# Performance work log

Hardware: AMD Instinct MI355X
Metric: run time of the kernel (lower is better)

The kernel has to match this reference:

```python
import jax, jax.numpy as jnp
import numpy as np

B, T, S, R, L = 16, 32, 512, 8, 256
H, E, V, NL = 512, 512, 50000, 3
OOV = 50


def setup_inputs() -> dict:
    key = jax.random.key(0)
    ks = jax.random.split(key, 40)
    p = lambda i, shape: jax.random.normal(ks[i], shape, dtype=jnp.float32) * 0.02
    d = {
        'tokens': jax.random.randint(ks[0], (B, T), 0, V),
        'src_oov': jax.random.randint(ks[1], (B, S), 0, V),
        'ref_oovs': jax.random.randint(ks[2], (B, R, L), 0, V),
        'src_mask': jnp.ones((B, S), bool),
        'ref_word_mask': jnp.ones((B, R, L), bool),
        'ref_doc_mask': jnp.ones((B, R), bool),
        'max_num_oov': OOV,
        'cur_word_rep': jax.random.normal(ks[3], (B, S, H), dtype=jnp.float32),
        'ref_word_reps': jax.random.normal(ks[4], (B, R, L, H), dtype=jnp.float32),
        'ref_doc_reps': jax.random.normal(ks[5], (B, R, H), dtype=jnp.float32),
        'hidden0': jax.random.normal(ks[6], (NL, B, H), dtype=jnp.float32),
        'embed_w': p(7, (V, E)),
        'gru_wih': p(8, (NL, 3 * H, H)),  # layer0 input dim E == H
        'gru_whh': p(9, (NL, 3 * H, H)),
        'gru_bih': p(10, (NL, 3 * H)),
        'gru_bhh': p(11, (NL, 3 * H)),
        'attn_Wd': p(12, (H, H)), 'attn_We': p(13, (H, H)), 'attn_v': p(14, (H,)),
        'hd_Wd': p(15, (H, H)), 'hd_We': p(16, (H, H)), 'hd_v': p(17, (H,)),
        'hw_Wd': p(18, (H, H)), 'hw_We': p(19, (H, H)), 'hw_v': p(20, (H,)),
        'gate_w': p(21, (2 * H, 1)), 'gate_b': p(22, (1,)),
        'fc_w': p(23, (2 * H, H)), 'fc_b': p(24, (H,)),
        'out_w': p(25, (H, V)), 'out_b': p(26, (V,)),
        'pgen_w': p(27, (E + 2 * H, 3)), 'pgen_b': p(28, (3,)),
    }
    return d


def _forward(embed_w, gru_wih, gru_whh, gru_bih, gru_bhh,
             attn_Wd, attn_We, attn_v, hd_Wd, hd_We, hd_v, hw_Wd, hw_We, hw_v,
             gate_w, gate_b, fc_w, fc_b, out_w, out_b, pgen_w, pgen_b,
             cur_word_rep, ref_word_reps, ref_doc_reps, hidden0,
             tokens, src_oov, ref_oovs, src_mask, ref_word_mask, ref_doc_mask,
             max_num_oov):
    b, t = tokens.shape
    x = embed_w[tokens]                               # [B,T,E]
    enc_proj = cur_word_rep @ attn_We                 # [B,S,H]
    doc_proj = ref_doc_reps @ hd_We                   # [B,R,H]
    word_proj = ref_word_reps @ hw_We                 # [B,R,L,H]
    NEG = jnp.float32(-1e9)

    def step(hidden, x_t):
        inp = x_t
        hs = []
        for l in range(hidden.shape[0]):
            gx = inp @ gru_wih[l].T + gru_bih[l]
            gh = hidden[l] @ gru_whh[l].T + gru_bhh[l]
            xr, xz, xn = jnp.split(gx, 3, -1)
            hr, hz, hn = jnp.split(gh, 3, -1)
            r = jax.nn.sigmoid(xr + hr)
            z = jax.nn.sigmoid(xz + hz)
            n = jnp.tanh(xn + r * hn)
            h = (1.0 - z) * n + z * hidden[l]
            hs.append(h)
            inp = h
        new_hidden = jnp.stack(hs)
        h_top = hs[-1]                                # [B,H]
        # additive attention over source words
        sc = jnp.tanh(enc_proj + (h_top @ attn_Wd)[:, None, :]) @ attn_v  # [B,S]
        aw = jax.nn.softmax(jnp.where(src_mask, sc, NEG), -1)
        ctx = jnp.einsum('bs,bsh->bh', aw, cur_word_rep)
        # hierarchical attention: doc level then word level
        scd = jnp.tanh(doc_proj + (h_top @ hd_Wd)[:, None, :]) @ hd_v     # [B,R]
        ad = jax.nn.softmax(jnp.where(ref_doc_mask, scd, NEG), -1)
        scw = jnp.tanh(word_proj + (h_top @ hw_Wd)[:, None, None, :]) @ hw_v  # [B,R,L]
        aww = jax.nn.softmax(jnp.where(ref_word_mask, scw, NEG), -1)
        ra = ad[:, :, None] * aww                     # [B,R,L]
        rctx = jnp.einsum('brl,brlh->bh', ra, ref_word_reps)
        # fusion gate
        g = jax.nn.sigmoid(jnp.concatenate([ctx, rctx], -1) @ gate_w + gate_b)  # [B,1]
        context = g * ctx + (1.0 - g) * rctx
        return new_hidden, (context, h_top, aw, ra)

    _, (contexts, hiddens, attn_dists, ref_attn_dists) = jax.lax.scan(
        step, hidden0, jnp.swapaxes(x, 0, 1))
    contexts = jnp.swapaxes(contexts, 0, 1)           # [B,T,H]
    hiddens = jnp.swapaxes(hiddens, 0, 1)             # [B,T,H]
    attn_dists = jnp.swapaxes(attn_dists, 0, 1)       # [B,T,S]
    ref_attn_dists = jnp.swapaxes(ref_attn_dists, 0, 1)  # [B,T,R,L]

    ch = jnp.concatenate([contexts, hiddens], -1)
    vocab_dist = jax.nn.softmax((ch @ fc_w + fc_b) @ out_w + out_b, -1)  # [B,T,V]
    pg = jax.nn.softmax(jnp.concatenate([contexts, hiddens, x], -1) @ pgen_w + pgen_b, -1)  # [B,T,3]
    vocab_dist_ = pg[..., 0:1] * vocab_dist
    attn_ = pg[..., 1:2] * attn_dists
    final = jnp.concatenate(
        [vocab_dist_, jnp.zeros((b, t, max_num_oov), vocab_dist_.dtype)], -1)
    bi = jnp.arange(b)[:, None, None]
    ti = jnp.arange(t)[None, :, None]
    idx = jnp.broadcast_to(src_oov[:, None, :], (b, t, src_oov.shape[-1]))
    final = final.at[bi, ti, idx].add(attn_)
    # multi-doc copy
    r, l = ref_oovs.shape[1], ref_oovs.shape[2]
    ref_attn_ = pg[..., 2][:, :, None, None] * ref_attn_dists
    ridx = jnp.broadcast_to(ref_oovs.reshape(b, 1, r * l), (b, t, r * l))
    final = final.at[bi, ti, ridx].add(ref_attn_.reshape(b, t, r * l))
    return final, attn_dists


def reference(tokens, src_oov, ref_oovs, src_mask, ref_word_mask, ref_doc_mask,
              max_num_oov, cur_word_rep, ref_word_reps, ref_doc_reps, hidden0,
              embed_w, gru_wih, gru_whh, gru_bih, gru_bhh,
              attn_Wd, attn_We, attn_v, hd_Wd, hd_We, hd_v, hw_Wd, hw_We, hw_v,
              gate_w, gate_b, fc_w, fc_b, out_w, out_b, pgen_w, pgen_b):
    return _forward(embed_w, gru_wih, gru_whh, gru_bih, gru_bhh,
                    attn_Wd, attn_We, attn_v, hd_Wd, hd_We, hd_v,
                    hw_Wd, hw_We, hw_v, gate_w, gate_b, fc_w, fc_b,
                    out_w, out_b, pgen_w, pgen_b,
                    cur_word_rep, ref_word_reps, ref_doc_reps, hidden0,
                    tokens, src_oov, ref_oovs, src_mask, ref_word_mask,
                    ref_doc_mask, max_num_oov)
```

## Files before the change

kernel.cpp:

```cpp
#include <hip/hip_runtime.h>
#include <hip/hip_bf16.h>


#define B_   16
#define T_   32
#define S_   512
#define R_   8
#define L_   256
#define RL_  2048
#define H_   512
#define V_   50000
#define NL_  3
#define OOV_ 50
#define M_   512
#define FINW 50050
#define S2C  2.8853900817779268f
#define GRUB 128
#define NCONV 128
#define HP16 520

typedef __attribute__((ext_vector_type(8))) short    short8;
typedef __attribute__((ext_vector_type(4))) float    f32x4;
typedef __attribute__((ext_vector_type(2))) _Float16 h2;
typedef __attribute__((ext_vector_type(8))) _Float16 h8;
// ... 32 lines not shown
__device__ __forceinline__ float dot8h(h8 w, h8 x, float acc){
#if __has_builtin(__builtin_amdgcn_fdot2)
  acc = __builtin_amdgcn_fdot2((h2){w[0], w[1]}, (h2){x[0], x[1]}, acc, false);
  acc = __builtin_amdgcn_fdot2((h2){w[2], w[3]}, (h2){x[2], x[3]}, acc, false);
  acc = __builtin_amdgcn_fdot2((h2){w[4], w[5]}, (h2){x[4], x[5]}, acc, false);
  acc = __builtin_amdgcn_fdot2((h2){w[6], w[7]}, (h2){x[6], x[7]}, acc, false);
#else
  #pragma unroll
  for (int q = 0; q < 8; q++) acc += (float)w[q] * (float)x[q];
#endif
  return acc;
}
__device__ __forceinline__ u64 allc(const u64* p){
  return __hip_atomic_load(p, __ATOMIC_RELAXED, __HIP_MEMORY_SCOPE_AGENT);
}
__device__ __forceinline__ float allcf(const float* p){
  u32 v = __hip_atomic_load((const u32*)p, __ATOMIC_RELAXED, __HIP_MEMORY_SCOPE_AGENT);
  union { u32 i; float f; } c; c.i = v; return c.f;
}


__global__ __launch_bounds__(256) void k_embed(const int* __restrict__ tokens,
                                               const float* __restrict__ embed_w,
                                               u16* __restrict__ x_bf){
  int rid = blockIdx.x;
  long tok = (long)tokens[rid];
  const float* src = embed_w + tok * H_;
  u16* dst = x_bf + (long)rid * H_;
  for (int e = threadIdx.x; e < H_; e += 256) dst[e] = f2bf(src[e]);
}

struct CJ { const float* s; u16* d; long n; int f16; };

__global__ __launch_bounds__(256) void k_conv6(CJ j0, CJ j1, CJ j2, CJ j3, CJ j4, CJ j5){
  int y = blockIdx.y;
  CJ j = (y == 0) ? j0 : (y == 1) ? j1 : (y == 2) ? j2 : (y == 3) ? j3 : (y == 4) ? j4 : j5;
  long n4 = j.n >> 2;
  long i = (long)blockIdx.x * 256 + threadIdx.x;
  long stride = (long)gridDim.x * 256;
  if (j.f16){
    for (; i < n4; i += stride){
      f32x4 v = *(const f32x4*)(j.s + 4 * i);
      u64 p = (u64)f2h(v[0]) | ((u64)f2h(v[1]) << 16)
            | ((u64)f2h(v[2]) << 32) | ((u64)f2h(v[3]) << 48);
      *(u64*)(j.d + 4 * i) = p;
    }
  } else {
    for (; i < n4; i += stride){
      f32x4 v = *(const f32x4*)(j.s + 4 * i);
      u64 p = (u64)f2bf(v[0]) | ((u64)f2bf(v[1]) << 16)
            | ((u64)f2bf(v[2]) << 32) | ((u64)f2bf(v[3]) << 48);
      *(u64*)(j.d + 4 * i) = p;
    }
  }
}

__global__ __launch_bounds__(256) void k_convT(const float* __restrict__ src, int Rr, int Cc,
                                               u16* __restrict__ dst){
  __shared__ float tile[32][33];
  int c0 = blockIdx.x * 32, r0 = blockIdx.y * 32;
  int tx = threadIdx.x & 31, ty = threadIdx.x >> 5;
  for (int i = ty; i < 32; i += 8){
    int r = r0 + i, c = c0 + tx;
    tile[i][tx] = (r < Rr && c < Cc) ? src[(long)r * Cc + c] : 0.f;
  }
  __syncthreads();
  for (int i = ty; i < 32; i += 8){
    int c = c0 + i, r = r0 + tx;
    if (c < Cc && r < Rr) dst[(long)c * Rr + r] = f2bf(tile[tx][i]);
  }
}

__global__ __launch_bounds__(256) void k_convT6(const float* s0, const float* s1,
    const float* s2, const float* s3, const float* s4, const float* s5,
    u16* __restrict__ dstb){
  int z = blockIdx.z;
  const float* src = (z == 0) ? s0 : (z == 1) ? s1 : (z == 2) ? s2
                   : (z == 3) ? s3 : (z == 4) ? s4 : s5;
  u16* dst = dstb + (long)z * H_ * H_;
  __shared__ float tile[32][33];
  int c0 = blockIdx.x * 32, r0 = blockIdx.y * 32;
  int tx = threadIdx.x & 31, ty = threadIdx.x >> 5;
  for (int i = ty; i < 32; i += 8)
    tile[i][tx] = src[(long)(r0 + i) * H_ + c0 + tx];
  __syncthreads();
  for (int i = ty; i < 32; i += 8)
// ... 149 lines not shown
  float mp = -1e30f;
  #pragma unroll 8
  for (int k = 0; k < 64; k += 2){
    float x0 = cbuf[rl][cbase + k], x1 = cbuf[rl][cbase + k + 1];
    float2 xy; xy.x = x0; xy.y = x1;
    *(float2*)(fin + gbase + k) = xy;
    if (cg + k < N)     mp = fmaxf(mp, x0);
    if (cg + k + 1 < N) mp = fmaxf(mp, x1);
  }
  float sp = 0.f;
  #pragma unroll 8
  for (int k = 0; k < 64; k++){
    if (cg + k < N) sp += __expf(cbuf[rl][cbase + k] - mp);
  }
  smx[rl][ch] = mp; ssx[rl][ch] = sp;
  __syncthreads();
  if (tid < 128){
    float ma = smx[tid][0], mb2 = smx[tid][1];
    float M = fmaxf(ma, mb2);
    float S = ssx[tid][0] * __expf(ma - M) + ssx[tid][1] * __expf(mb2 - M);
    long row = mb + tid;
    pm[row * 392 + blockIdx.y] = M;
    ps[row * 392 + blockIdx.y] = S;
  }
}


__global__ __launch_bounds__(512) void k_gru_mega(
    const float* __restrict__ gx0, const u16* __restrict__ wih_h,
    const u16* __restrict__ whh_h, const float* __restrict__ bih,
    const float* __restrict__ bhh, const float* __restrict__ hidden0,
    float* __restrict__ h_all, u16* __restrict__ ch_bf, unsigned int* cnt,
    const float* __restrict__ out_w, u16* __restrict__ outwT,
    const u16* __restrict__ cwr_bf, const u16* __restrict__ rwr_bf,
    const u16* __restrict__ rdr_bf, const u16* __restrict__ WT,
    u16* __restrict__ enc_bf, u16* __restrict__ wp_bf,
    float* __restrict__ doc_proj, int do_shadow){
  __shared__ u16 pH0[16][HP16], pH1[16][HP16], pX1[16][HP16], pH2[16][HP16], pX2[16][HP16];
  __shared__ float red0[8][3][4][16];
  __shared__ float red1[8][6][4][16];
  __shared__ float red2[8][6][4][16];
  __shared__ float tconv[2][32][33];
  int bid = blockIdx.x;
  int tid = threadIdx.x;

  if (bid >= GRUB){
    if (!do_shadow) return;
    int wid = bid - GRUB;
    int half = tid >> 8, t256 = tid & 255;
    int worker = wid * 2 + half;
    for (int tile = worker; tile < 1284; tile += 256){
      if (tile < 256)
        dev_gemm_tile(cwr_bf, H_, WT, H_, (const float*)0, (void*)enc_bf, H_,
                      H_, H_, 1, S2C, tile >> 2, tile & 3, t256);
      else if (tile < 1280){
        int t = tile - 256;
        dev_gemm_tile(rwr_bf, H_, WT + 2 * H_ * H_, H_, (const float*)0, (void*)wp_bf, H_,
                      H_, H_, 1, S2C, t >> 2, t & 3, t256);
      } else
        dev_gemm_tile(rdr_bf, H_, WT + H_ * H_, H_, (const float*)0, (void*)doc_proj, H_,
                      H_, H_, 0, S2C, 0, tile - 1280, t256);
    }
    __syncthreads();
    int sub = half, tx = t256 & 31, ty = t256 >> 5;
    const int NT = 1563 * 16;
    for (int base = wid * 2; base < NT; base += NCONV * 2){
      int tile = base + sub;
      bool act = tile < NT;
      int cx = act ? (tile % 1563) : 0;
      int ry = act ? (tile / 1563) : 0;
      int c0 = cx * 32, r0 = ry * 32;
      if (act){
        for (int i = ty; i < 32; i += 8){
          int c = c0 + tx;
          tconv[sub][i][tx] = (c < V_) ? out_w[(long)(r0 + i) * V_ + c] : 0.f;
        }
      }
      __syncthreads();
      if (act){
        for (int i = ty; i < 32; i += 8){
          int c = c0 + i;
          if (c < V_) outwT[(long)c * H_ + r0 + tx] = f2bf(tconv[sub][tx][i]);
        }
      }
      __syncthreads();
    }
    return;
  }

  int bx = bid;
  int b = tid & 15, jj = (tid >> 4) & 3, ks = tid >> 6;
  int j = bx * 4 + jj;
  int kbase = ks * 64;
  int srow = tid >> 5, sl32 = tid & 31;

  for (int s = 0; s < T_ + NL_ - 1; s++){
    int t0 = s, t1 = s - 1, t2v = s - 2;
    bool a0 = (t0 < T_);
    bool a1 = (t1 >= 0 && t1 < T_);
    bool a2 = (t2v >= 0 && t2v < T_);
    float hpj_r = 0.f, gx_r0 = 0.f, gx_r1 = 0.f, gx_r2 = 0.f;
    if (tid < 192){
      int lz = tid >> 6, b2 = tid & 15, jj2 = (tid >> 4) & 3;
      int j2 = bx * 4 + jj2;
      int tt = s - lz;
      if (tt >= 0 && tt < T_){
        hpj_r = (tt == 0) ? hidden0[(lz * B_ + b2) * H_ + j2]
                          : allcf(h_all + (long)((lz * T_ + tt - 1) * B_ + b2) * H_ + j2);
        if (lz == 0){
          const float* g = gx0 + (long)(b2 * T_ + tt) * 1536 + j2;
          gx_r0 = g[0]; gx_r1 = g[512]; gx_r2 = g[1024];
        }
      }
    }
    {
      u64 v;
      #define STAGE(PAN, ROWPTR, ATOMIC)                                         \
        {                                                                        \
          const u64* p = (const u64*)(ROWPTR);                                   \
          _Pragma("unroll")                                                      \
          for (int q = 0; q < 8; q++){                                           \
            v = (ATOMIC) ? allc(p + sl32 + 32 * q) : p[sl32 + 32 * q];           \
            union { u64 w; float f[2]; } uu; uu.w = v;                           \
            union { _Float16 h[2]; u32 u; } pk;                                  \
            pk.h[0] = (_Float16)uu.f[0]; pk.h[1] = (_Float16)uu.f[1];            \
            *(u32*)&PAN[srow][2 * (sl32 + 32 * q)] = pk.u;                       \
          }                                                                      \
        }
      if (a0){
        if (t0 == 0) STAGE(pH0, hidden0 + (long)(0 * B_ + srow) * H_, false)
        else         STAGE(pH0, h_all + (long)((0 * T_ + t0 - 1) * B_ + srow) * H_, true)
      }
      if (a1){
        if (t1 == 0) STAGE(pH1, hidden0 + (long)(1 * B_ + srow) * H_, false)
        else         STAGE(pH1, h_all + (long)((1 * T_ + t1 - 1) * B_ + srow) * H_, true)
        STAGE(pX1, h_all + (long)((0 * T_ + t1) * B_ + srow) * H_, true)
      }
      if (a2){
        if (t2v == 0) STAGE(pH2, hidden0 + (long)(2 * B_ + srow) * H_, false)
        else          STAGE(pH2, h_all + (long)((2 * T_ + t2v - 1) * B_ + srow) * H_, true)
        STAGE(pX2, h_all + (long)((1 * T_ + t2v) * B_ + srow) * H_, true)
      }
      #undef STAGE
    }
    __syncthreads();

    if (a0){
      const u16* wl = whh_h;
      const h8* w0 = (const h8*)(wl + ((long)(0 * H_ + j)) * H_ + kbase);
      const h8* w1 = (const h8*)(wl + ((long)(1 * H_ + j)) * H_ + kbase);
      const h8* w2 = (const h8*)(wl + ((long)(2 * H_ + j)) * H_ + kbase);
      float s0 = 0.f, s1 = 0.f, s2 = 0.f;
      #pragma unroll 2
      for (int k8 = 0; k8 < 8; k8++){
        h8 hv = *(const h8*)&pH0[b][kbase + 8 * k8];
        s0 = dot8h(w0[k8], hv, s0);
        s1 = dot8h(w1[k8], hv, s1);
        s2 = dot8h(w2[k8], hv, s2);
      }
      red0[ks][0][jj][b] = s0; red0[ks][1][jj][b] = s1; red0[ks][2][jj][b] = s2;
    }
    if (a1){
      const u16* wl = whh_h + (long)1 * 1536 * H_;
      const u16* ul = wih_h + (long)1 * 1536 * H_;
      const h8* w0 = (const h8*)(wl + ((long)(0 * H_ + j)) * H_ + kbase);
      const h8* w1 = (const h8*)(wl + ((long)(1 * H_ + j)) * H_ + kbase);
      const h8* w2 = (const h8*)(wl + ((long)(2 * H_ + j)) * H_ + kbase);
      const h8* u0 = (const h8*)(ul + ((long)(0 * H_ + j)) * H_ + kbase);
      const h8* u1 = (const h8*)(ul + ((long)(1 * H_ + j)) * H_ + kbase);
      const h8* u2 = (const h8*)(ul + ((long)(2 * H_ + j)) * H_ + kbase);
      float s0 = 0.f, s1 = 0.f, s2 = 0.f, x0 = 0.f, x1 = 0.f, x2 = 0.f;
      #pragma unroll 2
      for (int k8 = 0; k8 < 8; k8++){
        h8 hv = *(const h8*)&pH1[b][kbase + 8 * k8];
        h8 xv = *(const h8*)&pX1[b][kbase + 8 * k8];
        s0 = dot8h(w0[k8], hv, s0);
        s1 = dot8h(w1[k8], hv, s1);
        s2 = dot8h(w2[k8], hv, s2);
        x0 = dot8h(u0[k8], xv, x0);
        x1 = dot8h(u1[k8], xv, x1);
        x2 = dot8h(u2[k8], xv, x2);
      }
      red1[ks][0][jj][b] = s0; red1[ks][1][jj][b] = s1; red1[ks][2][jj][b] = s2;
      red1[ks][3][jj][b] = x0; red1[ks][4][jj][b] = x1; red1[ks][5][jj][b] = x2;
    }
    if (a2){
      const u16* wl = whh_h + (long)2 * 1536 * H_;
      const u16* ul = wih_h + (long)2 * 1536 * H_;
      const h8* w0 = (const h8*)(wl + ((long)(0 * H_ + j)) * H_ + kbase);
      const h8* w1 = (const h8*)(wl + ((long)(1 * H_ + j)) * H_ + kbase);
      const h8* w2 = (const h8*)(wl + ((long)(2 * H_ + j)) * H_ + kbase);
      const h8* u0 = (const h8*)(ul + ((long)(0 * H_ + j)) * H_ + kbase);
      const h8* u1 = (const h8*)(ul + ((long)(1 * H_ + j)) * H_ + kbase);
      const h8* u2 = (const h8*)(ul + ((long)(2 * H_ + j)) * H_ + kbase);
      float s0 = 0.f, s1 = 0.f, s2 = 0.f, x0 = 0.f, x1 = 0.f, x2 = 0.f;
      #pragma unroll 2
      for (int k8 = 0; k8 < 8; k8++){
        h8 hv = *(const h8*)&pH2[b][kbase + 8 * k8];
        h8 xv = *(const h8*)&pX2[b][kbase + 8 * k8];
        s0 = dot8h(w0[k8], hv, s0);
        s1 = dot8h(w1[k8], hv, s1);
        s2 = dot8h(w2[k8], hv, s2);
        x0 = dot8h(u0[k8], xv, x0);
        x1 = dot8h(u1[k8], xv, x1);
        x2 = dot8h(u2[k8], xv, x2);
      }
      red2[ks][0][jj][b] = s0; red2[ks][1][jj][b] = s1; red2[ks][2][jj][b] = s2;
      red2[ks][3][jj][b] = x0; red2[ks][4][jj][b] = x1; red2[ks][5][jj][b] = x2;
    }
    __syncthreads();

    if (tid < 192){
      int lz = tid >> 6, b2 = tid & 15, jj2 = (tid >> 4) & 3;
      int j2 = bx * 4 + jj2;
      int tt = s - lz;
      if (tt >= 0 && tt < T_){
        float gh[3], gxv[3];
        #pragma unroll
        for (int g = 0; g < 3; g++){
          float a = 0.f, c = 0.f;
          if (lz == 0){
            #pragma unroll
            for (int q = 0; q < 8; q++) a += red0[q][g][jj2][b2];
          } else if (lz == 1){
            #pragma unroll
            for (int q = 0; q < 8; q++){ a += red1[q][g][jj2][b2]; c += red1[q][3 + g][jj2][b2]; }
          } else {
            #pragma unroll
            for (int q = 0; q < 8; q++){ a += red2[q][g][jj2][b2]; c += red2[q][3 + g][jj2][b2]; }
          }
          gh[g] = a + bhh[lz * 1536 + g * H_ + j2];
          if (lz == 0) gxv[g] = (g == 0) ? gx_r0 : (g == 1) ? gx_r1 : gx_r2;
// ... 126 lines not shown
    if (tid == 0){
      float m = -1e30f;
      for (int q = 0; q < 8; q++) m = fmaxf(m, red8[q][0]);
      float e[8], sum = 0.f;
      for (int q = 0; q < 8; q++){ e[q] = __expf(red8[q][0] - m); sum += e[q]; }
      float inv = 1.f / sum;
      for (int q = 0; q < 8; q++) ad[rid * R_ + q] = e[q] * inv;
    }
  }
}

__global__ __launch_bounds__(256) void k_aww_ra(float* __restrict__ raBuf,
                                                const float* __restrict__ ad){
  int rid = blockIdx.x, r = blockIdx.y, tid = threadIdx.x;
  float* row = raBuf + (long)rid * RL_ + r * L_;
  float x = row[tid];
  float m = x;
  for (int o = 32; o > 0; o >>= 1) m = fmaxf(m, __shfl_xor(m, o));
  __shared__ float red[4];
  if ((tid & 63) == 0) red[tid >> 6] = m;
  __syncthreads();
  m = fmaxf(fmaxf(red[0], red[1]), fmaxf(red[2], red[3]));
  float e = __expf(x - m);
  float s = e;
  for (int o = 32; o > 0; o >>= 1) s += __shfl_xor(s, o);
  __syncthreads();
  if ((tid & 63) == 0) red[tid >> 6] = s;
  __syncthreads();
  s = red[0] + red[1] + red[2] + red[3];
  row[tid] = (e / s) * ad[rid * R_ + r];
}


__global__ __launch_bounds__(256) void k_awgemm(const float* __restrict__ wts, int KS, int CH,
    const u16* __restrict__ Wbuf, float* __restrict__ pdst){
  int b = blockIdx.x, ht = blockIdx.y, kc = blockIdx.z;
  int tid = threadIdx.x;
  int hl = tid & 63, tq = tid >> 6;
  int h = ht * 256 + hl * 4;
  int base = kc * CH;
  float a[8][4];
  #pragma unroll
  for (int tt = 0; tt < 8; tt++)
    #pragma unroll
    for (int q = 0; q < 4; q++) a[tt][q] = 0.f;
  const float* wrow = wts + ((long)(b * T_) + tq * 8) * KS + base;
  for (int sl = 0; sl < CH; sl++){
    const u16* wp = Wbuf + ((long)b * KS + base + sl) * H_ + h;
    u32 p0 = *(const u32*)(wp);
    u32 p1 = *(const u32*)(wp + 2);
    float v0 = bf2f((u16)(p0 & 0xffff)), v1 = bf2f((u16)(p0 >> 16));
    float v2 = bf2f((u16)(p1 & 0xffff)), v3 = bf2f((u16)(p1 >> 16));
    #pragma unroll
    for (int tt = 0; tt < 8; tt++){
      float w = wrow[(long)tt * KS + sl];
      a[tt][0] += w * v0; a[tt][1] += w * v1;
      a[tt][2] += w * v2; a[tt][3] += w * v3;
    }
  }
  #pragma unroll
  for (int tt = 0; tt < 8; tt++){
    long o = (long)kc * (2 * M_ * H_) + ((long)(b * T_ + tq * 8 + tt)) * H_ + h;
    *(f32x4*)(pdst + o) = (f32x4){a[tt][0], a[tt][1], a[tt][2], a[tt][3]};
  }
}

__global__ __launch_bounds__(256) void k_red8(const float* __restrict__ pbuf,
                                              float* __restrict__ outp){
  long n = 2L * M_ * H_;
// ... 28 lines not shown
    contexts[(long)rid * H_ + h] = v;
    ch_bf[(long)rid * 1024 + h] = f2bf(v);
  }
  float p0 = 0.f, p1 = 0.f, p2 = 0.f;
  for (int k = tid; k < 1536; k += 256){
    float v;
    if (k < 512)       v = g * c[k] + (1.f - g) * rc[k];
    else if (k < 1024) v = h_all[((2 * T_ + t) * B_ + b) * H_ + (k - 512)];
    else               v = bf2f(x_bf[(long)rid * H_ + (k - 1024)]);
    p0 += v * pgen_w[k * 3 + 0];
    p1 += v * pgen_w[k * 3 + 1];
    p2 += v * pgen_w[k * 3 + 2];
  }
  for (int o = 32; o > 0; o >>= 1){
    p0 += __shfl_xor(p0, o); p1 += __shfl_xor(p1, o); p2 += __shfl_xor(p2, o);
  }
  __shared__ float r0[4], r1[4], r2[4];
  if ((tid & 63) == 0){ r0[tid >> 6] = p0; r1[tid >> 6] = p1; r2[tid >> 6] = p2; }
  __syncthreads();
  if (tid == 0){
    p0 = r0[0]+r0[1]+r0[2]+r0[3] + pgen_b[0];
    p1 = r1[0]+r1[1]+r1[2]+r1[3] + pgen_b[1];
    p2 = r2[0]+r2[1]+r2[2]+r2[3] + pgen_b[2];
    float m = fmaxf(p0, fmaxf(p1, p2));
    float e0 = __expf(p0 - m), e1 = __expf(p1 - m), e2 = __expf(p2 - m);
    float inv = 1.f / (e0 + e1 + e2);
    pg[rid * 3 + 0] = e0 * inv;
    pg[rid * 3 + 1] = e1 * inv;
    pg[rid * 3 + 2] = e2 * inv;
  }
}


__global__ __launch_bounds__(256) void k_vred391(const float* __restrict__ pm,
    const float* __restrict__ ps, float* __restrict__ vmax, float* __restrict__ vsum){
  int rid = blockIdx.x, tid = threadIdx.x;
  const float* mrow = pm + (long)rid * 392;
  const float* srow = ps + (long)rid * 392;
  float m = -1e30f, s = 0.f;
  for (int q = tid; q < 391; q += 256){
    float m2 = mrow[q], s2 = srow[q];
    float M = fmaxf(m, m2);
    s = s * __expf(m - M) + s2 * __expf(m2 - M);
    m = M;
  }
  for (int o = 32; o > 0; o >>= 1){
    float m2 = __shfl_xor(m, o), s2 = __shfl_xor(s, o);
    float M = fmaxf(m, m2);
    s = s * __expf(m - M) + s2 * __expf(m2 - M);
    m = M;
  }
  __shared__ float rm[4], rs[4];
  if ((tid & 63) == 0){ rm[tid >> 6] = m; rs[tid >> 6] = s; }
  __syncthreads();
  if (tid == 0){
    float Mx = rm[0], Sx = rs[0];
    for (int q = 1; q < 4; q++){
      float M2 = fmaxf(Mx, rm[q]);
      Sx = Sx * __expf(Mx - M2) + rs[q] * __expf(rm[q] - M2);
      Mx = M2;
    }
    vmax[rid] = Mx; vsum[rid] = Sx;
  }
}

__global__ __launch_bounds__(256) void k_final_vocab(float* __restrict__ fin,
    const float* __restrict__ vmax, const float* __restrict__ vsum,
    const float* __restrict__ pg){
  int rid = blockIdx.y;
  int v = (blockIdx.x * 256 + threadIdx.x) * 2;
  if (v >= FINW) return;
  long base = (long)rid * FINW;
  float scale = pg[rid * 3 + 0] / vsum[rid];
  float mx = vmax[rid];
  if (v + 1 < V_){
    float2* p = (float2*)(fin + base + v);
    float2 x = *p;
    x.x = __expf(x.x - mx) * scale;
    x.y = __expf(x.y - mx) * scale;
    *p = x;
  } else {
    for (int q = 0; q < 2 && v + q < FINW; q++){
      float x = fin[base + v + q];
      fin[base + v + q] = (v + q < V_) ? __expf(x - mx) * scale : 0.f;
    }
  }
}

__global__ __launch_bounds__(256) void k_scatter_src(float* __restrict__ fin,
    const float* __restrict__ aw, const float* __restrict__ pg,
    const int* __restrict__ src_oov){
  int rid = blockIdx.x, tid = threadIdx.x;
  int b = rid / T_;
  float p1 = pg[rid * 3 + 1];
  for (int s = tid; s < S_; s += 256){
    float val = p1 * aw[(long)rid * S_ + s];
    int idx = src_oov[b * S_ + s];
    atomicAdd(fin + (long)rid * FINW + idx, val);
  }
}

__global__ __launch_bounds__(256) void k_scatter_ref(float* __restrict__ fin,
    const float* __restrict__ raBuf, const float* __restrict__ pg,
    const int* __restrict__ ref_oovs){
  int rid = blockIdx.x, tid = threadIdx.x;
  int b = rid / T_;
  float p2 = pg[rid * 3 + 2];
  for (int i = tid; i < RL_; i += 256){
    float val = p2 * raBuf[(long)rid * RL_ + i];
    int idx = ref_oovs[b * RL_ + i];
    atomicAdd(fin + (long)rid * FINW + idx, val);
  }
}


extern "C" void kernel_launch(void* const* d_in, const int* in_sizes, int n_in,
                              void* d_out, int out_size, void* d_ws, size_t ws_size,
                              hipStream_t stream)
{
  (void)in_sizes; (void)n_in; (void)out_size;
  const int*   tokens   = (const int*)  d_in[0];
  const int*   src_oov  = (const int*)  d_in[1];
  const int*   ref_oovs = (const int*)  d_in[2];
  const float* cwr      = (const float*)d_in[7];
  const float* rwr      = (const float*)d_in[8];
  const float* rdr      = (const float*)d_in[9];
  const float* hidden0  = (const float*)d_in[10];
  const float* embed_w  = (const float*)d_in[11];
  const float* gru_wih  = (const float*)d_in[12];
  const float* gru_whh  = (const float*)d_in[13];
  const float* gru_bih  = (const float*)d_in[14];
  const float* gru_bhh  = (const float*)d_in[15];
  const float* attn_Wd  = (const float*)d_in[16];
  const float* attn_We  = (const float*)d_in[17];
  const float* attn_v   = (const float*)d_in[18];
  const float* hd_Wd    = (const float*)d_in[19];
  const float* hd_We    = (const float*)d_in[20];
  const float* hd_v     = (const float*)d_in[21];
  const float* hw_Wd    = (const float*)d_in[22];
  const float* hw_We    = (const float*)d_in[23];
  const float* hw_v     = (const float*)d_in[24];
  const float* gate_w   = (const float*)d_in[25];
  const float* gate_b   = (const float*)d_in[26];
  const float* fc_w     = (const float*)d_in[27];
  const float* fc_b     = (const float*)d_in[28];
  const float* out_w    = (const float*)d_in[29];
  const float* out_b    = (const float*)d_in[30];
  const float* pgen_w   = (const float*)d_in[31];
  const float* pgen_b   = (const float*)d_in[32];

  float* fin = (float*)d_out;
  float* aw  = fin + (long)M_ * FINW;

  char* wptr = (char*)d_ws;
  auto alloc = [&](size_t nbytes) -> void* {
    void* p = (void*)wptr;
    wptr += (nbytes + 255) & ~(size_t)255;
    return p;
  };
  float* gx0      = (float*)alloc((size_t)M_ * 1536 * 4);
  float* h_all    = (float*)alloc((size_t)NL_ * T_ * B_ * H_ * 4);
  float* dec_all  = (float*)alloc((size_t)M_ * 1536 * 4);
  float* raBuf    = (float*)alloc((size_t)M_ * RL_ * 4);
  float* ad       = (float*)alloc((size_t)M_ * R_ * 4);
  float* ctx      = (float*)alloc((size_t)M_ * H_ * 4);
  float* rctx     = (float*)alloc((size_t)M_ * H_ * 4);
  float* contexts = (float*)alloc((size_t)M_ * H_ * 4);
  float* pg       = (float*)alloc((size_t)M_ * 3 * 4);
  float* vmax     = (float*)alloc((size_t)M_ * 4);
  float* vsum     = (float*)alloc((size_t)M_ * 4);
  float* pm       = (float*)alloc((size_t)M_ * 392 * 4);
  float* ps       = (float*)alloc((size_t)M_ * 392 * 4);
  float* doc_proj = (float*)alloc((size_t)B_ * R_ * H_ * 4);
  float* pbuf     = (float*)alloc((size_t)8 * 2 * M_ * H_ * 4);
  unsigned int* gru_cnt = (unsigned int*)alloc(GRUB * 16 * 4);
  u16* x_bf       = (u16*)alloc((size_t)M_ * H_ * 2);
  u16* ch_bf      = (u16*)alloc((size_t)M_ * 1024 * 2);
  u16* whh_h16    = (u16*)alloc((size_t)NL_ * 1536 * H_ * 2);
  u16* wih_h16    = (u16*)alloc((size_t)NL_ * 1536 * H_ * 2);
  u16* wih0_bf    = (u16*)alloc((size_t)1536 * H_ * 2);
  u16* WT         = (u16*)alloc((size_t)6 * H_ * H_ * 2);
  u16* fcwT       = (u16*)alloc((size_t)H_ * 1024 * 2);
  u16* fcout_bf   = (u16*)alloc((size_t)M_ * H_ * 2);
  u16* cwr_bf     = (u16*)alloc((size_t)B_ * S_ * H_ * 2);
  u16* enc_bf     = (u16*)alloc((size_t)B_ * S_ * H_ * 2);
  u16* rwr_bf     = (u16*)alloc((size_t)B_ * RL_ * H_ * 2);
  u16* wp_bf      = (u16*)alloc((size_t)B_ * RL_ * H_ * 2);
  u16* rdr_bf     = (u16*)alloc((size_t)B_ * R_ * H_ * 2);
  u16* outwT_ded  = (u16*)alloc((size_t)V_ * H_ * 2);
  bool big = ((char*)outwT_ded + (size_t)V_ * H_ * 2) <= ((char*)d_ws + ws_size);
  u16* outwT = big ? outwT_ded : rwr_bf;
  int nshadow = big ? NCONV : 0;

  hipMemsetAsync(gru_cnt, 0, GRUB * 16 * 4, stream);

  k_embed<<<M_, 256, 0, stream>>>(tokens, embed_w, x_bf);
  {
    CJ j0{cwr, cwr_bf, (long)B_ * S_ * H_, 0};
    CJ j1{rwr, rwr_bf, (long)B_ * RL_ * H_, 0};
    CJ j2{gru_whh, whh_h16, (long)NL_ * 1536 * H_, 1};
    CJ j3{gru_wih, wih_h16, (long)NL_ * 1536 * H_, 1};
    CJ j4{rdr, rdr_bf, (long)B_ * R_ * H_, 0};
    CJ j5{gru_wih, wih0_bf, (long)1536 * H_, 0};
    k_conv6<<<dim3(512, 6), 256, 0, stream>>>(j0, j1, j2, j3, j4, j5);
  }
  k_convT6<<<dim3(16, 16, 6), 256, 0, stream>>>(attn_We, hd_We, hw_We,
                                                attn_Wd, hd_Wd, hw_Wd, WT);
  k_convT<<<dim3(16, 32), 256, 0, stream>>>(fc_w, 1024, H_, fcwT);

  k_gemm_nt<<<dim3(4, 12), 256, 0, stream>>>(x_bf, H_, wih0_bf, H_, gru_bih,
                                             (void*)gx0, 1536, 1536, H_, 0, 1.f);
  if (!big){
    k_gemm_nt<<<dim3(64, 4), 256, 0, stream>>>(cwr_bf, H_, WT, H_, (const float*)0,
                                               (void*)enc_bf, H_, H_, H_, 1, S2C);
    k_gemm_nt<<<dim3(256, 4), 256, 0, stream>>>(rwr_bf, H_, WT + 2 * H_ * H_, H_, (const float*)0,
                                                (void*)wp_bf, H_, H_, H_, 1, S2C);
    k_gemm_nt<<<dim3(1, 4), 256, 0, stream>>>(rdr_bf, H_, WT + H_ * H_, H_, (const float*)0,
                                              (void*)doc_proj, H_, H_, H_, 0, S2C);
  }

  k_gru_mega<<<GRUB + nshadow, 512, 0, stream>>>(gx0, wih_h16, whh_h16, gru_bih, gru_bhh,
                                                 hidden0, h_all, ch_bf, gru_cnt,
                                                 out_w, outwT, cwr_bf, rwr_bf, rdr_bf,
                                                 WT, enc_bf, wp_bf, doc_proj, big ? 1 : 0);

  k_gemm_nt<<<dim3(4, 12), 256, 0, stream>>>(ch_bf + 512, 1024, WT + 3 * H_ * H_, H_,
                                             (const float*)0, (void*)dec_all, 1536, 1536, H_, 0, S2C);

  k_scores2<<<dim3(16, 40, 4), 256, 0, stream>>>(enc_bf, wp_bf, dec_all, attn_v, hw_v, aw, raBuf);
  k_smax_scd<<<dim3(M_, 2), 256, 0, stream>>>(aw, doc_proj, dec_all, hd_v, ad);
  k_aww_ra<<<dim3(M_, R_), 256, 0, stream>>>(raBuf, ad);

  k_awgemm<<<dim3(B_, 2, 8), 256, 0, stream>>>(aw, S_, 64, cwr_bf, pbuf);
  k_awgemm<<<dim3(B_, 2, 8), 256, 0, stream>>>(raBuf, RL_, 256, rwr_bf, pbuf + (long)M_ * H_);
  if (!big)
    k_convT<<<dim3(1563, 16), 256, 0, stream>>>(out_w, H_, V_, outwT);
  k_red8<<<(2 * M_ * H_ + 255) / 256, 256, 0, stream>>>(pbuf, ctx);

  k_gatepgen<<<M_, 256, 0, stream>>>(ctx, rctx, gate_w, gate_b, contexts, ch_bf,
                                     h_all, x_bf, pgen_w, pgen_b, pg);

  k_gemm_nt<<<dim3(4, 4), 256, 0, stream>>>(ch_bf, 1024, fcwT, 1024, fc_b,
                                            (void*)fcout_bf, H_, H_, 1024, 1, 1.f);
  k_gemm_out<<<dim3(4, 391), 256, 0, stream>>>(fcout_bf, outwT, out_b, fin, pm, ps);
  k_vred391<<<M_, 256, 0, stream>>>(pm, ps, vmax, vsum);
  k_final_vocab<<<dim3(98, M_), 256, 0, stream>>>(fin, vmax, vsum, pg);
  k_scatter_src<<<M_, 256, 0, stream>>>(fin, aw, pg, src_oov);
  k_scatter_ref<<<M_, 256, 0, stream>>>(fin, raBuf, pg, ref_oovs);
}
```

Baseline: 1.148 ms.

## Move input conversions into GRU shadow blocks and fuse several small kernels

The bf16 conversion of cur/ref word reps and the transposes of the attention and fc weights move into the shadow blocks of the GRU megakernel, which run alongside the recurrence. A grid-wide flag barrier among the shadow blocks then gates the projection GEMMs. The GRU staging now reuses each layer's input panel as the next layer's hidden panel, cutting shared memory and redundant loads. The two awgemm launches, the vred391 and final-vocab kernels, and the two scatter kernels are each merged into one, trading extra launches for recomputing the softmax stats in every block of a row. The spin barrier assumes all shadow blocks are co-resident, and its guard counter can let blocks continue before the conversions finish.

```diff
diff --git a/kernel.cpp b/kernel.cpp
--- a/kernel.cpp
+++ b/kernel.cpp
@@ -88,9 +88,9 @@
 
 struct CJ { const float* s; u16* d; long n; int f16; };
 
-__global__ __launch_bounds__(256) void k_conv6(CJ j0, CJ j1, CJ j2, CJ j3, CJ j4, CJ j5){
+__global__ __launch_bounds__(256) void k_conv4(CJ j0, CJ j1, CJ j2, CJ j3){
   int y = blockIdx.y;
-  CJ j = (y == 0) ? j0 : (y == 1) ? j1 : (y == 2) ? j2 : (y == 3) ? j3 : (y == 4) ? j4 : j5;
+  CJ j = (y == 0) ? j0 : (y == 1) ? j1 : (y == 2) ? j2 : j3;
   long n4 = j.n >> 2;
   long i = (long)blockIdx.x * 256 + threadIdx.x;
   long stride = (long)gridDim.x * 256;
@@ -108,6 +108,20 @@
             | ((u64)f2bf(v[2]) << 32) | ((u64)f2bf(v[3]) << 48);
       *(u64*)(j.d + 4 * i) = p;
     }
+  }
+}
+
+__global__ __launch_bounds__(256) void k_conv2(CJ j0, CJ j1){
+  int y = blockIdx.y;
+  CJ j = (y == 0) ? j0 : j1;
+  long n4 = j.n >> 2;
+  long i = (long)blockIdx.x * 256 + threadIdx.x;
+  long stride = (long)gridDim.x * 256;
+  for (; i < n4; i += stride){
+    f32x4 v = *(const f32x4*)(j.s + 4 * i);
+    u64 p = (u64)f2bf(v[0]) | ((u64)f2bf(v[1]) << 16)
+          | ((u64)f2bf(v[2]) << 32) | ((u64)f2bf(v[3]) << 48);
+    *(u64*)(j.d + 4 * i) = p;
   }
 }
 
@@ -323,11 +337,16 @@
     const float* __restrict__ bhh, const float* __restrict__ hidden0,
     float* __restrict__ h_all, u16* __restrict__ ch_bf, unsigned int* cnt,
     const float* __restrict__ out_w, u16* __restrict__ outwT,
-    const u16* __restrict__ cwr_bf, const u16* __restrict__ rwr_bf,
-    const u16* __restrict__ rdr_bf, const u16* __restrict__ WT,
+    const float* __restrict__ cwr, const float* __restrict__ rwr,
+    u16* __restrict__ cwr_bf, u16* __restrict__ rwr_bf,
+    const u16* __restrict__ rdr_bf, u16* __restrict__ WT, u16* __restrict__ fcwT,
+    const float* __restrict__ wsrc0, const float* __restrict__ wsrc1,
+    const float* __restrict__ wsrc2, const float* __restrict__ wsrc3,
+    const float* __restrict__ wsrc4, const float* __restrict__ wsrc5,
+    const float* __restrict__ fc_w,
     u16* __restrict__ enc_bf, u16* __restrict__ wp_bf,
     float* __restrict__ doc_proj, int do_shadow){
-  __shared__ u16 pH0[16][HP16], pH1[16][HP16], pX1[16][HP16], pH2[16][HP16], pX2[16][HP16];
+  __shared__ u16 P0[16][HP16], P1[16][HP16], P2[16][HP16];
   __shared__ float red0[8][3][4][16];
   __shared__ float red1[8][6][4][16];
   __shared__ float red2[8][6][4][16];
@@ -339,42 +358,105 @@
     if (!do_shadow) return;
     int wid = bid - GRUB;
     int half = tid >> 8, t256 = tid & 255;
-    int worker = wid * 2 + half;
-    for (int tile = worker; tile < 1284; tile += 256){
-      if (tile < 256)
-        dev_gemm_tile(cwr_bf, H_, WT, H_, (const float*)0, (void*)enc_bf, H_,
-                      H_, H_, 1, S2C, tile >> 2, tile & 3, t256);
-      else if (tile < 1280){
-        int t = tile - 256;
-        dev_gemm_tile(rwr_bf, H_, WT + 2 * H_ * H_, H_, (const float*)0, (void*)wp_bf, H_,
-                      H_, H_, 1, S2C, t >> 2, t & 3, t256);
-      } else
-        dev_gemm_tile(rdr_bf, H_, WT + H_ * H_, H_, (const float*)0, (void*)doc_proj, H_,
-                      H_, H_, 0, S2C, 0, tile - 1280, t256);
-    }
-    __syncthreads();
-    int sub = half, tx = t256 & 31, ty = t256 >> 5;
-    const int NT = 1563 * 16;
-    for (int base = wid * 2; base < NT; base += NCONV * 2){
-      int tile = base + sub;
-      bool act = tile < NT;
-      int cx = act ? (tile % 1563) : 0;
-      int ry = act ? (tile / 1563) : 0;
-      int c0 = cx * 32, r0 = ry * 32;
-      if (act){
-        for (int i = ty; i < 32; i += 8){
-          int c = c0 + tx;
-          tconv[sub][i][tx] = (c < V_) ? out_w[(long)(r0 + i) * V_ + c] : 0.f;
+    {
+      long ncwr4 = ((long)B_ * S_ * H_) >> 2;
+      long nrwr4 = ((long)B_ * RL_ * H_) >> 2;
+      long tot4 = ncwr4 + nrwr4;
+      long idx = (long)wid * 512 + tid;
+      long stride = (long)NCONV * 512;
+      for (long i = idx; i < tot4; i += stride){
+        const float* s; u16* d; long off;
+        if (i < ncwr4){ s = cwr; d = cwr_bf; off = i; }
+        else          { s = rwr; d = rwr_bf; off = i - ncwr4; }
+        f32x4 v = *(const f32x4*)(s + 4 * off);
+        u64 p = (u64)f2bf(v[0]) | ((u64)f2bf(v[1]) << 16)
+              | ((u64)f2bf(v[2]) << 32) | ((u64)f2bf(v[3]) << 48);
+        *(u64*)(d + 4 * off) = p;
+      }
+    }
+    {
+      int sub = half, tx = t256 & 31, ty = t256 >> 5;
+      for (int base = wid * 2; base < 2048; base += NCONV * 2){
+        int tile = base + sub;
+        bool act = tile < 2048;
+        const float* src = wsrc0; u16* dst = WT; int Rr = 512, Cc = 512, r0 = 0, c0 = 0;
+        if (act){
+          if (tile < 1536){
+            int mat = tile >> 8, tt = tile & 255;
+            src = (mat == 0) ? wsrc0 : (mat == 1) ? wsrc1 : (mat == 2) ? wsrc2
+                : (mat == 3) ? wsrc3 : (mat == 4) ? wsrc4 : wsrc5;
+            dst = WT + (long)mat * H_ * H_;
+            Rr = 512; Cc = 512;
+            c0 = (tt & 15) * 32; r0 = (tt >> 4) * 32;
+          } else {
+            int tt = tile - 1536;
+            src = fc_w; dst = fcwT; Rr = 1024; Cc = 512;
+            c0 = (tt & 15) * 32; r0 = (tt >> 4) * 32;
+          }
+          for (int i = ty; i < 32; i += 8)
+            tconv[sub][i][tx] = src[(long)(r0 + i) * Cc + c0 + tx];
         }
-      }
-      __syncthreads();
-      if (act){
-        for (int i = ty; i < 32; i += 8){
-          int c = c0 + i;
-          if (c < V_) outwT[(long)c * H_ + r0 + tx] = f2bf(tconv[sub][tx][i]);
+        __syncthreads();
+        if (act){
+          for (int i = ty; i < 32; i += 8)
+            dst[(long)(c0 + i) * Rr + r0 + tx] = f2bf(tconv[sub][tx][i]);
         }
-      }
-      __syncthreads();
+        __syncthreads();
+      }
+    }
+    __syncthreads();
+    if (tid == 0)
+      __hip_atomic_store(cnt + (GRUB + wid) * 16, 1u,
+                         __ATOMIC_RELAXED, __HIP_MEMORY_SCOPE_AGENT);
+    if (tid < NCONV){
+      long guard = 0;
+      while (__hip_atomic_load(cnt + (GRUB + tid) * 16, __ATOMIC_RELAXED,
+                               __HIP_MEMORY_SCOPE_AGENT) < 1u && guard < (1L << 23)){
+        __builtin_amdgcn_s_sleep(1);
+        guard++;
+      }
+    }
+    __syncthreads();
+    {
+      int worker = wid * 2 + half;
+      for (int tile = worker; tile < 1284; tile += 256){
+        if (tile < 256)
+          dev_gemm_tile(cwr_bf, H_, WT, H_, (const float*)0, (void*)enc_bf, H_,
+                        H_, H_, 1, S2C, tile >> 2, tile & 3, t256);
+        else if (tile < 1280){
+          int t = tile - 256;
+          dev_gemm_tile(rwr_bf, H_, WT + 2 * H_ * H_, H_, (const float*)0, (void*)wp_bf, H_,
+                        H_, H_, 1, S2C, t >> 2, t & 3, t256);
+        } else
+          dev_gemm_tile(rdr_bf, H_, WT + H_ * H_, H_, (const float*)0, (void*)doc_proj, H_,
+                        H_, H_, 0, S2C, 0, tile - 1280, t256);
+      }
+    }
+    __syncthreads();
+    {
+      int sub = half, tx = t256 & 31, ty = t256 >> 5;
+      const int NT = 1563 * 16;
+      for (int base = wid * 2; base < NT; base += NCONV * 2){
+        int tile = base + sub;
+        bool act = tile < NT;
+        int cx = act ? (tile % 1563) : 0;
+        int ry = act ? (tile / 1563) : 0;
+        int c0 = cx * 32, r0 = ry * 32;
+        if (act){
+          for (int i = ty; i < 32; i += 8){
+            int c = c0 + tx;
+            tconv[sub][i][tx] = (c < V_) ? out_w[(long)(r0 + i) * V_ + c] : 0.f;
+          }
+        }
+        __syncthreads();
+        if (act){
+          for (int i = ty; i < 32; i += 8){
+            int c = c0 + i;
+            if (c < V_) outwT[(long)c * H_ + r0 + tx] = f2bf(tconv[sub][tx][i]);
+          }
+        }
+        __syncthreads();
+      }
     }
     return;
   }
@@ -418,19 +500,13 @@
             *(u32*)&PAN[srow][2 * (sl32 + 32 * q)] = pk.u;                       \
           }                                                                      \
         }
-      if (a0){
-        if (t0 == 0) STAGE(pH0, hidden0 + (long)(0 * B_ + srow) * H_, false)
-        else         STAGE(pH0, h_all + (long)((0 * T_ + t0 - 1) * B_ + srow) * H_, true)
-      }
-      if (a1){
-        if (t1 == 0) STAGE(pH1, hidden0 + (long)(1 * B_ + srow) * H_, false)
-        else         STAGE(pH1, h_all + (long)((1 * T_ + t1 - 1) * B_ + srow) * H_, true)
-        STAGE(pX1, h_all + (long)((0 * T_ + t1) * B_ + srow) * H_, true)
-      }
+      if (a0 && t0 == 0)      STAGE(P0, hidden0 + (long)(0 * B_ + srow) * H_, false)
+      else if (a0 || a1)      STAGE(P0, h_all + (long)((0 * T_ + s - 1) * B_ + srow) * H_, true)
+      if (a1 && t1 == 0)      STAGE(P1, hidden0 + (long)(1 * B_ + srow) * H_, false)
+      else if (a1 || a2)      STAGE(P1, h_all + (long)((1 * T_ + s - 2) * B_ + srow) * H_, true)
       if (a2){
-        if (t2v == 0) STAGE(pH2, hidden0 + (long)(2 * B_ + srow) * H_, false)
-        else          STAGE(pH2, h_all + (long)((2 * T_ + t2v - 1) * B_ + srow) * H_, true)
-        STAGE(pX2, h_all + (long)((1 * T_ + t2v) * B_ + srow) * H_, true)
+        if (t2v == 0)         STAGE(P2, hidden0 + (long)(2 * B_ + srow) * H_, false)
+        else                  STAGE(P2, h_all + (long)((2 * T_ + s - 3) * B_ + srow) * H_, true)
       }
       #undef STAGE
     }
@@ -444,7 +520,7 @@
       float s0 = 0.f, s1 = 0.f, s2 = 0.f;
       #pragma unroll 2
       for (int k8 = 0; k8 < 8; k8++){
-        h8 hv = *(const h8*)&pH0[b][kbase + 8 * k8];
+        h8 hv = *(const h8*)&P0[b][kbase + 8 * k8];
         s0 = dot8h(w0[k8], hv, s0);
         s1 = dot8h(w1[k8], hv, s1);
         s2 = dot8h(w2[k8], hv, s2);
@@ -463,8 +539,8 @@
       float s0 = 0.f, s1 = 0.f, s2 = 0.f, x0 = 0.f, x1 = 0.f, x2 = 0.f;
       #pragma unroll 2
       for (int k8 = 0; k8 < 8; k8++){
-        h8 hv = *(const h8*)&pH1[b][kbase + 8 * k8];
-        h8 xv = *(const h8*)&pX1[b][kbase + 8 * k8];
+        h8 hv = *(const h8*)&P1[b][kbase + 8 * k8];
+        h8 xv = *(const h8*)&P0[b][kbase + 8 * k8];
         s0 = dot8h(w0[k8], hv, s0);
         s1 = dot8h(w1[k8], hv, s1);
         s2 = dot8h(w2[k8], hv, s2);
@@ -487,8 +563,8 @@
       float s0 = 0.f, s1 = 0.f, s2 = 0.f, x0 = 0.f, x1 = 0.f, x2 = 0.f;
       #pragma unroll 2
       for (int k8 = 0; k8 < 8; k8++){
-        h8 hv = *(const h8*)&pH2[b][kbase + 8 * k8];
-        h8 xv = *(const h8*)&pX2[b][kbase + 8 * k8];
+        h8 hv = *(const h8*)&P2[b][kbase + 8 * k8];
+        h8 xv = *(const h8*)&P1[b][kbase + 8 * k8];
         s0 = dot8h(w0[k8], hv, s0);
         s1 = dot8h(w1[k8], hv, s1);
         s2 = dot8h(w2[k8], hv, s2);
@@ -681,9 +757,13 @@
 }
 
 
-__global__ __launch_bounds__(256) void k_awgemm(const float* __restrict__ wts, int KS, int CH,
-    const u16* __restrict__ Wbuf, float* __restrict__ pdst){
-  int b = blockIdx.x, ht = blockIdx.y, kc = blockIdx.z;
+__global__ __launch_bounds__(256) void k_awgemm2(const float* __restrict__ aw,
+    const float* __restrict__ raBuf, const u16* __restrict__ cwr_bf,
+    const u16* __restrict__ rwr_bf, float* __restrict__ pbuf){
+  int b = blockIdx.x, ht = blockIdx.y, z = blockIdx.z;
+  const float* wts; const u16* Wbuf; float* pdst; int KS, CH, kc;
+  if (z < 8){ wts = aw;    Wbuf = cwr_bf; pdst = pbuf;               KS = S_;  CH = 64;  kc = z; }
+  else      { wts = raBuf; Wbuf = rwr_bf; pdst = pbuf + (long)M_ * H_; KS = RL_; CH = 256; kc = z - 8; }
   int tid = threadIdx.x;
   int hl = tid & 63, tq = tid >> 6;
   int h = ht * 256 + hl * 4;
@@ -778,9 +858,10 @@
 }
 
 
-__global__ __launch_bounds__(256) void k_vred391(const float* __restrict__ pm,
-    const float* __restrict__ ps, float* __restrict__ vmax, float* __restrict__ vsum){
-  int rid = blockIdx.x, tid = threadIdx.x;
+__global__ __launch_bounds__(256) void k_final_vocab(float* __restrict__ fin,
+    const float* __restrict__ pm, const float* __restrict__ ps,
+    const float* __restrict__ pg){
+  int rid = blockIdx.y, tid = threadIdx.x;
   const float* mrow = pm + (long)rid * 392;
   const float* srow = ps + (long)rid * 392;
   float m = -1e30f, s = 0.f;
@@ -796,7 +877,7 @@
     s = s * __expf(m - M) + s2 * __expf(m2 - M);
     m = M;
   }
-  __shared__ float rm[4], rs[4];
+  __shared__ float rm[4], rs[4], fm, fs;
   if ((tid & 63) == 0){ rm[tid >> 6] = m; rs[tid >> 6] = s; }
   __syncthreads();
   if (tid == 0){
@@ -806,19 +887,14 @@
       Sx = Sx * __expf(Mx - M2) + rs[q] * __expf(rm[q] - M2);
       Mx = M2;
     }
-    vmax[rid] = Mx; vsum[rid] = Sx;
-  }
-}
-
-__global__ __launch_bounds__(256) void k_final_vocab(float* __restrict__ fin,
-    const float* __restrict__ vmax, const float* __restrict__ vsum,
-    const float* __restrict__ pg){
-  int rid = blockIdx.y;
-  int v = (blockIdx.x * 256 + threadIdx.x) * 2;
+    fm = Mx; fs = Sx;
+  }
+  __syncthreads();
+  float mx = fm;
+  float scale = pg[rid * 3 + 0] / fs;
+  int v = (blockIdx.x * 256 + tid) * 2;
   if (v >= FINW) return;
   long base = (long)rid * FINW;
-  float scale = pg[rid * 3 + 0] / vsum[rid];
-  float mx = vmax[rid];
   if (v + 1 < V_){
     float2* p = (float2*)(fin + base + v);
     float2 x = *p;
@@ -833,29 +909,27 @@
   }
 }
 
-__global__ __launch_bounds__(256) void k_scatter_src(float* __restrict__ fin,
-    const float* __restrict__ aw, const float* __restrict__ pg,
-    const int* __restrict__ src_oov){
-  int rid = blockIdx.x, tid = threadIdx.x;
-  int b = rid / T_;
-  float p1 = pg[rid * 3 + 1];
-  for (int s = tid; s < S_; s += 256){
-    float val = p1 * aw[(long)rid * S_ + s];
-    int idx = src_oov[b * S_ + s];
-    atomicAdd(fin + (long)rid * FINW + idx, val);
-  }
-}
-
-__global__ __launch_bounds__(256) void k_scatter_ref(float* __restrict__ fin,
-    const float* __restrict__ raBuf, const float* __restrict__ pg,
+__global__ __launch_bounds__(512) void k_scatter(float* __restrict__ fin,
+    const float* __restrict__ aw, const float* __restrict__ raBuf,
+    const float* __restrict__ pg, const int* __restrict__ src_oov,
     const int* __restrict__ ref_oovs){
   int rid = blockIdx.x, tid = threadIdx.x;
   int b = rid / T_;
-  float p2 = pg[rid * 3 + 2];
-  for (int i = tid; i < RL_; i += 256){
-    float val = p2 * raBuf[(long)rid * RL_ + i];
-    int idx = ref_oovs[b * RL_ + i];
-    atomicAdd(fin + (long)rid * FINW + idx, val);
+  if (tid < 256){
+    float p1 = pg[rid * 3 + 1];
+    for (int s = tid; s < S_; s += 256){
+      float val = p1 * aw[(long)rid * S_ + s];
+      int idx = src_oov[b * S_ + s];
+      atomicAdd(fin + (long)rid * FINW + idx, val);
+    }
+  } else {
+    int t2 = tid - 256;
+    float p2 = pg[rid * 3 + 2];
+    for (int i = t2; i < RL_; i += 256){
+      float val = p2 * raBuf[(long)rid * RL_ + i];
+      int idx = ref_oovs[b * RL_ + i];
+      atomicAdd(fin + (long)rid * FINW + idx, val);
+    }
   }
 }
 
@@ -913,13 +987,11 @@
   float* rctx     = (float*)alloc((size_t)M_ * H_ * 4);
   float* contexts = (float*)alloc((size_t)M_ * H_ * 4);
   float* pg       = (float*)alloc((size_t)M_ * 3 * 4);
-  float* vmax     = (float*)alloc((size_t)M_ * 4);
-  float* vsum     = (float*)alloc((size_t)M_ * 4);
   float* pm       = (float*)alloc((size_t)M_ * 392 * 4);
   float* ps       = (float*)alloc((size_t)M_ * 392 * 4);
   float* doc_proj = (float*)alloc((size_t)B_ * R_ * H_ * 4);
   float* pbuf     = (float*)alloc((size_t)8 * 2 * M_ * H_ * 4);
-  unsigned int* gru_cnt = (unsigned int*)alloc(GRUB * 16 * 4);
+  unsigned int* gru_cnt = (unsigned int*)alloc((GRUB + NCONV) * 16 * 4);
   u16* x_bf       = (u16*)alloc((size_t)M_ * H_ * 2);
   u16* ch_bf      = (u16*)alloc((size_t)M_ * 1024 * 2);
   u16* whh_h16    = (u16*)alloc((size_t)NL_ * 1536 * H_ * 2);
@@ -938,21 +1010,24 @@
   u16* outwT = big ? outwT_ded : rwr_bf;
   int nshadow = big ? NCONV : 0;
 
-  hipMemsetAsync(gru_cnt, 0, GRUB * 16 * 4, stream);
+  hipMemsetAsync(gru_cnt, 0, (GRUB + NCONV) * 16 * 4, stream);
 
   k_embed<<<M_, 256, 0, stream>>>(tokens, embed_w, x_bf);
   {
+    CJ j0{gru_whh, whh_h16, (long)NL_ * 1536 * H_, 1};
+    CJ j1{gru_wih, wih_h16, (long)NL_ * 1536 * H_, 1};
+    CJ j2{gru_wih, wih0_bf, (long)1536 * H_, 0};
+    CJ j3{rdr, rdr_bf, (long)B_ * R_ * H_, 0};
+    k_conv4<<<dim3(256, 4), 256, 0, stream>>>(j0, j1, j2, j3);
+  }
+  if (!big){
     CJ j0{cwr, cwr_bf, (long)B_ * S_ * H_, 0};
     CJ j1{rwr, rwr_bf, (long)B_ * RL_ * H_, 0};
-    CJ j2{gru_whh, whh_h16, (long)NL_ * 1536 * H_, 1};
-    CJ j3{gru_wih, wih_h16, (long)NL_ * 1536 * H_, 1};
-    CJ j4{rdr, rdr_bf, (long)B_ * R_ * H_, 0};
-    CJ j5{gru_wih, wih0_bf, (long)1536 * H_, 0};
-    k_conv6<<<dim3(512, 6), 256, 0, stream>>>(j0, j1, j2, j3, j4, j5);
-  }
-  k_convT6<<<dim3(16, 16, 6), 256, 0, stream>>>(attn_We, hd_We, hw_We,
-                                                attn_Wd, hd_Wd, hw_Wd, WT);
-  k_convT<<<dim3(16, 32), 256, 0, stream>>>(fc_w, 1024, H_, fcwT);
+    k_conv2<<<dim3(512, 2), 256, 0, stream>>>(j0, j1);
+    k_convT6<<<dim3(16, 16, 6), 256, 0, stream>>>(attn_We, hd_We, hw_We,
+                                                  attn_Wd, hd_Wd, hw_Wd, WT);
+    k_convT<<<dim3(16, 32), 256, 0, stream>>>(fc_w, 1024, H_, fcwT);
+  }
 
   k_gemm_nt<<<dim3(4, 12), 256, 0, stream>>>(x_bf, H_, wih0_bf, H_, gru_bih,
                                              (void*)gx0, 1536, 1536, H_, 0, 1.f);
@@ -967,8 +1042,10 @@
 
   k_gru_mega<<<GRUB + nshadow, 512, 0, stream>>>(gx0, wih_h16, whh_h16, gru_bih, gru_bhh,
                                                  hidden0, h_all, ch_bf, gru_cnt,
-                                                 out_w, outwT, cwr_bf, rwr_bf, rdr_bf,
-                                                 WT, enc_bf, wp_bf, doc_proj, big ? 1 : 0);
+                                                 out_w, outwT, cwr, rwr, cwr_bf, rwr_bf,
+                                                 rdr_bf, WT, fcwT,
+                                                 attn_We, hd_We, hw_We, attn_Wd, hd_Wd, hw_Wd,
+                                                 fc_w, enc_bf, wp_bf, doc_proj, big ? 1 : 0);
 
   k_gemm_nt<<<dim3(4, 12), 256, 0, stream>>>(ch_bf + 512, 1024, WT + 3 * H_ * H_, H_,
                                              (const float*)0, (void*)dec_all, 1536, 1536, H_, 0, S2C);
@@ -977,8 +1054,7 @@
   k_smax_scd<<<dim3(M_, 2), 256, 0, stream>>>(aw, doc_proj, dec_all, hd_v, ad);
   k_aww_ra<<<dim3(M_, R_), 256, 0, stream>>>(raBuf, ad);
 
-  k_awgemm<<<dim3(B_, 2, 8), 256, 0, stream>>>(aw, S_, 64, cwr_bf, pbuf);
-  k_awgemm<<<dim3(B_, 2, 8), 256, 0, stream>>>(raBuf, RL_, 256, rwr_bf, pbuf + (long)M_ * H_);
+  k_awgemm2<<<dim3(B_, 2, 16), 256, 0, stream>>>(aw, raBuf, cwr_bf, rwr_bf, pbuf);
   if (!big)
     k_convT<<<dim3(1563, 16), 256, 0, stream>>>(out_w, H_, V_, outwT);
   k_red8<<<(2 * M_ * H_ + 255) / 256, 256, 0, stream>>>(pbuf, ctx);
@@ -989,8 +1065,6 @@
   k_gemm_nt<<<dim3(4, 4), 256, 0, stream>>>(ch_bf, 1024, fcwT, 1024, fc_b,
                                             (void*)fcout_bf, H_, H_, 1024, 1, 1.f);
   k_gemm_out<<<dim3(4, 391), 256, 0, stream>>>(fcout_bf, outwT, out_b, fin, pm, ps);
-  k_vred391<<<M_, 256, 0, stream>>>(pm, ps, vmax, vsum);
-  k_final_vocab<<<dim3(98, M_), 256, 0, stream>>>(fin, vmax, vsum, pg);
-  k_scatter_src<<<M_, 256, 0, stream>>>(fin, aw, pg, src_oov);
-  k_scatter_ref<<<M_, 256, 0, stream>>>(fin, raBuf, pg, ref_oovs);
-}
+  k_final_vocab<<<dim3(98, M_), 256, 0, stream>>>(fin, pm, ps, pg);
+  k_scatter<<<M_, 512, 0, stream>>>(fin, aw, raBuf, pg, src_oov, ref_oovs);
+}
```

After: 1.157 ms. Within noise of the previous version (+0.8%).
